# Optimization experiments

Measured on AMD Instinct MI355X. Metric: run time of the kernel, lower is better.

The kernel has to match this reference:

```python
import jax, jax.numpy as jnp
import numpy as np

B, T, C = 32, 4096, 128  # batch, TRAIN_LEN, channels (= nb_filters)
K, D = 3, 8              # kernel_size, dilation_rate
F = 128                  # nb_filters


def my_deconv1d(x, kernel, bias, dilation):
    """Faithful MyDeConv1D: dilated transposed conv via scatter-add.

    Original: raw[b,t,k,f] = sum_c(x[b,t,c]*W[c,k,f] + bias[f])
              => einsum + C_in*bias (bias added before the C-sum!).
    Then each raw[b,t,j,:] contributes to output position t + j*d,
    summed over t (gather_nd + double reduce_sum), keep last T steps.
    """
    b, t_len, c_in = x.shape
    _, k_size, f_out = kernel.shape
    raw = jnp.einsum('btc,ckf->btkf', x, kernel) + c_in * bias  # (B,T,K,F)
    final_len = t_len + (k_size - 1) * dilation
    pos = (jnp.arange(t_len)[:, None] + jnp.arange(k_size)[None, :] * dilation).reshape(-1)  # (T*K,)
    out = jnp.zeros((b, final_len, f_out), x.dtype)
    out = out.at[:, pos, :].add(raw.reshape(b, t_len * k_size, f_out))
    return out[:, -t_len:, :]


def setup_inputs() -> dict:
    key = jax.random.key(0)
    k1, k2, k3, k4, k5 = jax.random.split(key, 5)
    he = lambda k, shape, fan_in: jax.random.normal(k, shape, jnp.float32) * np.sqrt(2.0 / fan_in)
    return {
        'x': jax.random.normal(k1, (B, T, C), jnp.float32),
        'kernel1': he(k2, (C, K, F), C * K),
        'bias1': jnp.zeros((F,), jnp.float32),
        'kernel2': he(k3, (F, K, F), F * K),
        'bias2': jnp.zeros((F,), jnp.float32),
    }


def reference(x, kernel1, bias1, kernel2, bias2):
    # TemporalDeConvBlock: repeat_times=2, residual=True, norm_way=None,
    # dropout_rate=0 (identity), activation='relu', identity shape-match.
    h = jax.nn.relu(my_deconv1d(x, kernel1, bias1, D))
    h = jax.nn.relu(my_deconv1d(h, kernel2, bias2, D))
    return jax.nn.relu(h + x)
```

## Files before the change

### kernel.cpp

```cpp
#include <hip/hip_runtime.h>
#include <hip/hip_fp16.h>

#define BATCH 32
#define TLEN  4096
#define CH    128
#define KW    3
#define DIL   8

#define BM    64
#define HROWS (BM + 2 * DIL)
#define XROWS (BM + 4 * DIL)
#define LDSC  132

typedef _Float16 f16x8 __attribute__((ext_vector_type(8)));
typedef float    f32x4 __attribute__((ext_vector_type(4)));

__global__ void prep_weights_kernel(const float* __restrict__ W1,
                                    const float* __restrict__ W2,
                                    _Float16* __restrict__ Wt1,
                                    _Float16* __restrict__ Wt2) {
    const int total = KW * CH * CH;
    int idx = blockIdx.x * 256 + threadIdx.x;
    if (idx >= 2 * total) return;
    const float* W  = (idx < total) ? W1 : W2;
    _Float16*    Wt = (idx < total) ? Wt1 : Wt2;
    int r = idx % total;
    int j = r / (CH * CH);
    int f = (r / CH) % CH;
    int c = r % CH;
    Wt[j * CH * CH + f * CH + c] = (_Float16)W[c * (KW * CH) + j * CH + f];
}

__global__ __launch_bounds__(512, 4)
void fused_deconv_kernel(const float* __restrict__ x,
                         const _Float16* __restrict__ Wt1,
                         const float* __restrict__ bias1,
                         const _Float16* __restrict__ Wt2,
                         const float* __restrict__ bias2,
                         float* __restrict__ out)
{
    __shared__ __align__(16) _Float16 buf[XROWS][LDSC];

    const int tid  = threadIdx.x;
    const int lane = tid & 63;
    const int wid  = tid >> 6;
    const int l15  = lane & 15;
    const int kg   = lane >> 4;
    const int nc   = wid << 4;

    const int bt = blockIdx.x;
    const int b  = bt >> 6;
    const int t0 = (bt & 63) << 6;

    f16x8 w1[12];
#pragma unroll
    for (int ks = 0; ks < 12; ++ks) {
        const int j  = ks >> 2;
        const int c0 = (ks & 3) << 5;
        w1[ks] = *(const f16x8*)(Wt1 + (size_t)j * (CH * CH)
                                 + (nc + l15) * CH + c0 + kg * 8);
    }

    for (int i = tid; i < XROWS * 16; i += 512) {
        const int row = i >> 4;
        const int c8  = (i & 15) << 3;
        const int t   = t0 + row;
        f16x8 o;
        if (t < TLEN) {
            const float* xp = x + ((size_t)b * TLEN + t) * CH + c8;
            f32x4 v0 = *(const f32x4*)(xp + 0);
            f32x4 v1 = *(const f32x4*)(xp + 4);
            o[0] = (_Float16)v0[0]; o[1] = (_Float16)v0[1];
            o[2] = (_Float16)v0[2]; o[3] = (_Float16)v0[3];
            o[4] = (_Float16)v1[0]; o[5] = (_Float16)v1[1];
            o[6] = (_Float16)v1[2]; o[7] = (_Float16)v1[3];
        } else {
            o = (f16x8){};
        }
        *(f16x8*)&buf[row][c8] = o;
    }

    const float bv1 = 128.0f * bias1[nc + l15];
    const float bv2 = 128.0f * bias2[nc + l15];

    __syncthreads();

    f32x4 acc1[5];
#pragma unroll
    for (int m = 0; m < 5; ++m) acc1[m] = (f32x4){0.f, 0.f, 0.f, 0.f};
#pragma unroll
    for (int ks = 0; ks < 12; ++ks) {
        const int j     = ks >> 2;
        const int c0    = (ks & 3) << 5;
        const int shift = (2 - j) * DIL;
#pragma unroll
        for (int m = 0; m < 5; ++m) {
            f16x8 af = *(const f16x8*)&buf[m * 16 + shift + l15][c0 + kg * 8];
            acc1[m] = __builtin_amdgcn_mfma_f32_16x16x32_f16(af, w1[ks], acc1[m], 0, 0, 0);
        }
    }

    f16x8 w2[12];
#pragma unroll
    for (int ks = 0; ks < 12; ++ks) {
        const int j  = ks >> 2;
        const int c0 = (ks & 3) << 5;
        w2[ks] = *(const f16x8*)(Wt2 + (size_t)j * (CH * CH)
                                 + (nc + l15) * CH + c0 + kg * 8);
    }

    __syncthreads();

    {
        const int f = nc + l15;
#pragma unroll
        for (int m = 0; m < 5; ++m) {
#pragma unroll
            for (int i = 0; i < 4; ++i) {
                const int r = m * 16 + kg * 4 + i;
                const int u = t0 + r;
                const int nv = 1 + (u < TLEN - DIL) + (u < TLEN - 2 * DIL);
                float v = acc1[m][i] + (float)nv * bv1;
                v = fmaxf(v, 0.0f);
                buf[r][f] = (u < TLEN) ? (_Float16)v : (_Float16)0.0f;
            }
        }
    }
    __syncthreads();

    f32x4 acc2[4];
#pragma unroll
    for (int m = 0; m < 4; ++m) acc2[m] = (f32x4){0.f, 0.f, 0.f, 0.f};
#pragma unroll
    for (int ks = 0; ks < 12; ++ks) {
        const int j     = ks >> 2;
        const int c0    = (ks & 3) << 5;
        const int shift = (2 - j) * DIL;
#pragma unroll
        for (int m = 0; m < 4; ++m) {
            f16x8 af = *(const f16x8*)&buf[m * 16 + shift + l15][c0 + kg * 8];
            acc2[m] = __builtin_amdgcn_mfma_f32_16x16x32_f16(af, w2[ks], acc2[m], 0, 0, 0);
        }
    }

    {
        const int f = nc + l15;
#pragma unroll
        for (int m = 0; m < 4; ++m) {
#pragma unroll
            for (int i = 0; i < 4; ++i) {
                const int r = m * 16 + kg * 4 + i;
                const int t = t0 + r;
                const int nv = 1 + (t < TLEN - DIL) + (t < TLEN - 2 * DIL);
                float v = acc2[m][i] + (float)nv * bv2;
                v = fmaxf(v, 0.0f);
                const size_t gi = ((size_t)b * TLEN + t) * CH + f;
                v = v + x[gi];
                v = fmaxf(v, 0.0f);
                out[gi] = v;
            }
        }
    }
}

extern "C" void kernel_launch(void* const* d_in, const int* in_sizes, int n_in,
                              void* d_out, int out_size, void* d_ws, size_t ws_size,
                              hipStream_t stream) {
    const float* x  = (const float*)d_in[0];
    const float* W1 = (const float*)d_in[1];
    const float* b1 = (const float*)d_in[2];
    const float* W2 = (const float*)d_in[3];
    const float* b2 = (const float*)d_in[4];
    float* out = (float*)d_out;

    _Float16* Wt1 = (_Float16*)d_ws;
    _Float16* Wt2 = Wt1 + KW * CH * CH;

    prep_weights_kernel<<<(2 * KW * CH * CH + 255) / 256, 256, 0, stream>>>(W1, W2, Wt1, Wt2);

    const int grid = BATCH * (TLEN / BM);
    fused_deconv_kernel<<<grid, 512, 0, stream>>>(x, Wt1, b1, Wt2, b2, out);
}
```

Measured before the change: 77.30 us.

## Double time tile to 128 rows and batch x loads into registers

Raises the per-block time tile from 64 to 128 rows, so the dilated halo recomputation of the first layer (extra rows) is amortized over more output rows and the grid is halved. Global loads of x are now issued all at once into registers before converting to fp16 and storing to LDS, increasing memory-level parallelism. LDS row padding changes from 132 to 136. The cost is more accumulator and staging registers (9+8 accumulators, 40 floats of staged x) and more LDS per block, which may reduce occupancy under the 512x4 launch bound and lowers the block count to 1024.

```diff
diff --git a/kernel.cpp b/kernel.cpp
--- a/kernel.cpp
+++ b/kernel.cpp
@@ -7,10 +7,10 @@
 #define KW    3
 #define DIL   8
 
-#define BM    64
-#define HROWS (BM + 2 * DIL)
-#define XROWS (BM + 4 * DIL)
-#define LDSC  132
+#define BM    128
+#define HR    (BM + 2 * DIL)
+#define WROWS (BM + 4 * DIL)
+#define LDSC  136
 
 typedef _Float16 f16x8 __attribute__((ext_vector_type(8)));
 typedef float    f32x4 __attribute__((ext_vector_type(4)));
@@ -39,7 +39,7 @@
                          const float* __restrict__ bias2,
                          float* __restrict__ out)
 {
-    __shared__ __align__(16) _Float16 buf[XROWS][LDSC];
+    __shared__ __align__(16) _Float16 buf[WROWS][LDSC];
 
     const int tid  = threadIdx.x;
     const int lane = tid & 63;
@@ -49,8 +49,8 @@
     const int nc   = wid << 4;
 
     const int bt = blockIdx.x;
-    const int b  = bt >> 6;
-    const int t0 = (bt & 63) << 6;
+    const int b  = bt >> 5;
+    const int t0 = (bt & 31) << 7;
 
     f16x8 w1[12];
 #pragma unroll
@@ -61,22 +61,32 @@
                                  + (nc + l15) * CH + c0 + kg * 8);
     }
 
-    for (int i = tid; i < XROWS * 16; i += 512) {
+    f32x4 va[5][2];
+#pragma unroll
+    for (int p = 0; p < 5; ++p) {
+        const int i   = tid + 512 * p;
         const int row = i >> 4;
         const int c8  = (i & 15) << 3;
         const int t   = t0 + row;
-        f16x8 o;
         if (t < TLEN) {
             const float* xp = x + ((size_t)b * TLEN + t) * CH + c8;
-            f32x4 v0 = *(const f32x4*)(xp + 0);
-            f32x4 v1 = *(const f32x4*)(xp + 4);
-            o[0] = (_Float16)v0[0]; o[1] = (_Float16)v0[1];
-            o[2] = (_Float16)v0[2]; o[3] = (_Float16)v0[3];
-            o[4] = (_Float16)v1[0]; o[5] = (_Float16)v1[1];
-            o[6] = (_Float16)v1[2]; o[7] = (_Float16)v1[3];
+            va[p][0] = *(const f32x4*)(xp + 0);
+            va[p][1] = *(const f32x4*)(xp + 4);
         } else {
-            o = (f16x8){};
+            va[p][0] = (f32x4){0.f, 0.f, 0.f, 0.f};
+            va[p][1] = (f32x4){0.f, 0.f, 0.f, 0.f};
         }
+    }
+#pragma unroll
+    for (int p = 0; p < 5; ++p) {
+        const int i   = tid + 512 * p;
+        const int row = i >> 4;
+        const int c8  = (i & 15) << 3;
+        f16x8 o;
+        o[0] = (_Float16)va[p][0][0]; o[1] = (_Float16)va[p][0][1];
+        o[2] = (_Float16)va[p][0][2]; o[3] = (_Float16)va[p][0][3];
+        o[4] = (_Float16)va[p][1][0]; o[5] = (_Float16)va[p][1][1];
+        o[6] = (_Float16)va[p][1][2]; o[7] = (_Float16)va[p][1][3];
         *(f16x8*)&buf[row][c8] = o;
     }
 
@@ -85,16 +95,16 @@
 
     __syncthreads();
 
-    f32x4 acc1[5];
+    f32x4 acc1[9];
 #pragma unroll
-    for (int m = 0; m < 5; ++m) acc1[m] = (f32x4){0.f, 0.f, 0.f, 0.f};
+    for (int m = 0; m < 9; ++m) acc1[m] = (f32x4){0.f, 0.f, 0.f, 0.f};
 #pragma unroll
     for (int ks = 0; ks < 12; ++ks) {
         const int j     = ks >> 2;
         const int c0    = (ks & 3) << 5;
         const int shift = (2 - j) * DIL;
 #pragma unroll
-        for (int m = 0; m < 5; ++m) {
+        for (int m = 0; m < 9; ++m) {
             f16x8 af = *(const f16x8*)&buf[m * 16 + shift + l15][c0 + kg * 8];
             acc1[m] = __builtin_amdgcn_mfma_f32_16x16x32_f16(af, w1[ks], acc1[m], 0, 0, 0);
         }
@@ -114,7 +124,7 @@
     {
         const int f = nc + l15;
 #pragma unroll
-        for (int m = 0; m < 5; ++m) {
+        for (int m = 0; m < 9; ++m) {
 #pragma unroll
             for (int i = 0; i < 4; ++i) {
                 const int r = m * 16 + kg * 4 + i;
@@ -128,16 +138,16 @@
     }
     __syncthreads();
 
-    f32x4 acc2[4];
+    f32x4 acc2[8];
 #pragma unroll
-    for (int m = 0; m < 4; ++m) acc2[m] = (f32x4){0.f, 0.f, 0.f, 0.f};
+    for (int m = 0; m < 8; ++m) acc2[m] = (f32x4){0.f, 0.f, 0.f, 0.f};
 #pragma unroll
     for (int ks = 0; ks < 12; ++ks) {
         const int j     = ks >> 2;
         const int c0    = (ks & 3) << 5;
         const int shift = (2 - j) * DIL;
 #pragma unroll
-        for (int m = 0; m < 4; ++m) {
+        for (int m = 0; m < 8; ++m) {
             f16x8 af = *(const f16x8*)&buf[m * 16 + shift + l15][c0 + kg * 8];
             acc2[m] = __builtin_amdgcn_mfma_f32_16x16x32_f16(af, w2[ks], acc2[m], 0, 0, 0);
         }
@@ -146,7 +156,7 @@
     {
         const int f = nc + l15;
 #pragma unroll
-        for (int m = 0; m < 4; ++m) {
+        for (int m = 0; m < 8; ++m) {
 #pragma unroll
             for (int i = 0; i < 4; ++i) {
                 const int r = m * 16 + kg * 4 + i;
```

Result: slower. 144.6 us (+87.1%).
